# Kernel tuning notes

Hardware: AMD Instinct MI355X
Metric: run time of the kernel (lower is better)

Reference implementation:

```python
import jax, jax.numpy as jnp
import numpy as np

NUM_HEADS = 32
ROPE_BASE = 10000.0


def _rotate_half(x):
    h = x.shape[-1] // 2
    return jnp.concatenate([-x[..., h:], x[..., :h]], axis=-1)


def setup_inputs() -> dict:
    key = jax.random.key(0)
    ks = jax.random.split(key, 6)
    B, S, H = 2, 2048, 4096
    hidden_states = jax.random.normal(ks[0], (B, S, H), dtype=jnp.float32)
    # additive causal mask: 0 on/below diagonal, large negative above
    causal = jnp.tril(jnp.ones((S, S), dtype=bool))
    attention_mask = jnp.where(causal, 0.0, -1e9).astype(jnp.float32)
    attention_mask = jnp.broadcast_to(attention_mask[None, None], (B, 1, S, S))
    position_ids = jnp.broadcast_to(jnp.arange(S, dtype=jnp.int64 if jax.config.jax_enable_x64 else jnp.int32)[None, :], (B, S))
    scale = 1.0 / np.sqrt(H)
    Wq = jax.random.normal(ks[1], (H, H), dtype=jnp.float32) * scale
    Wk = jax.random.normal(ks[2], (H, H), dtype=jnp.float32) * scale
    Wv = jax.random.normal(ks[3], (H, H), dtype=jnp.float32) * scale
    Wo = jax.random.normal(ks[4], (H, H), dtype=jnp.float32) * scale
    return {"hidden_states": hidden_states, "attention_mask": attention_mask,
            "position_ids": position_ids, "Wq": Wq, "Wk": Wk, "Wv": Wv, "Wo": Wo}


def reference(hidden_states, attention_mask, position_ids, Wq, Wk, Wv, Wo):
    B, S, H = hidden_states.shape
    nh = NUM_HEADS
    hd = H // nh
    # QKV projections (torch Linear: y = x @ W.T), split heads -> [B, nh, S, hd]
    def proj(W):
        y = jnp.einsum('bsh,oh->bso', hidden_states, W)
        return y.reshape(B, S, nh, hd).transpose(0, 2, 1, 3)
    q, k, v = proj(Wq), proj(Wk), proj(Wv)
    # rotary embeddings gathered at position_ids
    inv_freq = 1.0 / (ROPE_BASE ** (jnp.arange(0, hd, 2, dtype=jnp.float32) / hd))
    freqs = position_ids.astype(jnp.float32)[:, :, None] * inv_freq[None, None, :]  # [B,S,hd/2]
    emb = jnp.concatenate([freqs, freqs], axis=-1)  # [B,S,hd]
    cos = jnp.cos(emb)[:, None, :, :]  # [B,1,S,hd]
    sin = jnp.sin(emb)[:, None, :, :]
    q = q * cos + _rotate_half(q) * sin
    k = k * cos + _rotate_half(k) * sin
    # scaled dot-product attention
    scores = jnp.einsum('bhqd,bhkd->bhqk', q, k) / jnp.sqrt(jnp.float32(hd))
    scores = scores + attention_mask
    scores = jnp.maximum(scores, jnp.finfo(scores.dtype).min)
    attn = jax.nn.softmax(scores, axis=-1)
    out = jnp.einsum('bhqk,bhkd->bhqd', attn, v)  # [B,nh,S,hd]
    out = out.transpose(0, 2, 1, 3).reshape(B, S, H)
    return jnp.einsum('bsh,oh->bso', out, Wo)
```

## Files before the change

### kernel.cpp

```cpp
#include <hip/hip_runtime.h>
#include <cstdint>
#include <cmath>

typedef __bf16 bf16;
typedef __bf16 bf16x8 __attribute__((ext_vector_type(8)));
typedef __bf16 bf16x4 __attribute__((ext_vector_type(4)));
typedef float f32x4 __attribute__((ext_vector_type(4)));

#define B_ 2
#define S_ 2048
#define H_ 4096
#define NH 32
#define HD 128

#define VMCNT(n) asm volatile("s_waitcnt vmcnt(" #n ")" ::: "memory")
#define BAR() __builtin_amdgcn_s_barrier()

__device__ __forceinline__ void gl_lds16(const void* g, void* l) {
  __builtin_amdgcn_global_load_lds(
      (const __attribute__((address_space(1))) unsigned int*)g,
      (__attribute__((address_space(3))) unsigned int*)l, 16, 0, 0);
}

__global__ __launch_bounds__(256) void cast_kernel(const float* __restrict__ in,
                                                   bf16* __restrict__ out, int n4) {
  int i = blockIdx.x * 256 + threadIdx.x;
  if (i < n4) {
    float4 v = ((const float4*)in)[i];
    bf16x4 o = {(bf16)v.x, (bf16)v.y, (bf16)v.z, (bf16)v.w};
    ((bf16x4*)out)[i] = o;
  }
}

template <int TM, int TN>
__device__ __forceinline__ void mfma_q(f32x4 (&acc)[8][4], bf16x8 (&a)[4][2],
                                       bf16x8 (&b)[2][2]) {
  __builtin_amdgcn_s_setprio(1);
#pragma unroll
  for (int i = 0; i < 4; ++i)
#pragma unroll
    for (int j = 0; j < 2; ++j)
#pragma unroll
      for (int kf = 0; kf < 2; ++kf)
        acc[TM * 4 + i][TN * 2 + j] = __builtin_amdgcn_mfma_f32_16x16x32_bf16(
            a[i][kf], b[j][kf], acc[TM * 4 + i][TN * 2 + j], 0, 0, 0);
  __builtin_amdgcn_s_setprio(0);
}

template <int EPI>
__global__ __launch_bounds__(512, 2) void gemm256(const bf16* __restrict__ A,
                                                  const bf16* __restrict__ Bw,
                                                  void* __restrict__ Cout) {
  constexpr int K = 4096, N = 4096, KT = K / 64;
  __shared__ __attribute__((aligned(16))) char lds[131072];
  char* Al = lds;
  char* Bl = lds + 65536;
  int tid = threadIdx.x;
  int l = tid & 63, lr = l & 15, lg = l >> 4;
  int w = tid >> 6, wm = w >> 2, wn = w & 3;
  int bid = (int)blockIdx.x;
  int swb = (bid & 7) * 32 + (bid >> 3);
  int r0 = (swb >> 4) * 256, c0 = (swb & 15) * 256;
  const bf16* Ab = A + (size_t)r0 * K;
  const bf16* Bb = Bw + (size_t)c0 * K;

  int lr0 = tid >> 3;
  int cel = (((tid & 7) ^ ((tid >> 3) & 7)) << 3);

  auto stageA = [&](int buf, int mh, int k0) {
    char* dst = Al + buf * 32768 + mh * 16384 + tid * 16;
    int ra = mh * 64 + lr0;
    gl_lds16(Ab + (size_t)ra * K + k0 + cel, dst);
    gl_lds16(Ab + (size_t)(ra + 128) * K + k0 + cel, dst + 8192);
  };
  auto stageB = [&](int buf, int nh, int k0) {
    char* dst = Bl + buf * 32768 + nh * 16384 + tid * 16;
    int n0 = (lr0 >> 5) * 64 + nh * 32 + (lr0 & 31);
    gl_lds16(Bb + (size_t)n0 * K + k0 + cel, dst);
    gl_lds16(Bb + (size_t)(n0 + 128) * K + k0 + cel, dst + 8192);
  };

  int rsw = (lr & 7) << 4;
  auto ldA = [&](bf16x8 (&dst)[4][2], int buf, int mh) {
    char* base = Al + buf * 32768 + mh * 16384 + wm * 8192;
#pragma unroll
    for (int mfl = 0; mfl < 4; ++mfl)
#pragma unroll
      for (int kf = 0; kf < 2; ++kf)
        __builtin_memcpy(&dst[mfl][kf],
                         base + (mfl * 16 + lr) * 128 + ((kf * 64 + lg * 16) ^ rsw), 16);
  };
  auto ldB = [&](bf16x8 (&dst)[2][2], int buf, int nh) {
    char* base = Bl + buf * 32768 + nh * 16384 + wn * 4096;
#pragma unroll
    for (int nfl = 0; nfl < 2; ++nfl)
#pragma unroll
      for (int kf = 0; kf < 2; ++kf)
        __builtin_memcpy(&dst[nfl][kf],
                         base + (nfl * 16 + lr) * 128 + ((kf * 64 + lg * 16) ^ rsw), 16);
  };

  bf16x8 af[4][2], bf0[2][2], bf1[2][2];
  f32x4 acc[8][4] = {};

  stageA(0, 0, 0);
  stageB(0, 0, 0);
  stageB(0, 1, 0);
  stageA(0, 1, 0);
  VMCNT(4); BAR();

  for (int kt = 0; kt < KT - 1; ++kt) {
    int buf = kt & 1, nb = buf ^ 1;
    int k0n = (kt + 1) * 64;
    ldA(af, buf, 0);
    ldB(bf0, buf, 0);
    stageA(nb, 0, k0n);
    mfma_q<0, 0>(acc, af, bf0);
    VMCNT(2); BAR();
    ldB(bf1, buf, 1);
    stageB(nb, 0, k0n);
    mfma_q<0, 1>(acc, af, bf1);
    ldA(af, buf, 1);
    stageB(nb, 1, k0n);
    mfma_q<1, 1>(acc, af, bf1);
    stageA(nb, 1, k0n);
    mfma_q<1, 0>(acc, af, bf0);
    VMCNT(4); BAR();
  }
  {
    int buf = (KT - 1) & 1;
    ldA(af, buf, 0);
    ldB(bf0, buf, 0);
    mfma_q<0, 0>(acc, af, bf0);
    VMCNT(2); BAR();
    ldB(bf1, buf, 1);
    mfma_q<0, 1>(acc, af, bf1);
    VMCNT(0); BAR();
    ldA(af, buf, 1);
    mfma_q<1, 1>(acc, af, bf1);
    mfma_q<1, 0>(acc, af, bf0);
  }

#pragma unroll
  for (int mf = 0; mf < 8; ++mf)
#pragma unroll
    for (int nf = 0; nf < 4; ++nf) {
      int orow = r0 + wm * 128 + mf * 16 + lg * 4;
      int ocol = c0 + wn * 64 + nf * 16 + lr;
      if (EPI == 0) {
        bf16* C = (bf16*)Cout;
#pragma unroll
        for (int jr = 0; jr < 4; ++jr)
          C[(size_t)(orow + jr) * N + ocol] = (bf16)acc[mf][nf][jr];
      } else {
        float* C = (float*)Cout;
#pragma unroll
        for (int jr = 0; jr < 4; ++jr)
          C[(size_t)(orow + jr) * N + ocol] = acc[mf][nf][jr];
      }
    }
}

__global__ __launch_bounds__(256) void rope_kernel(bf16* __restrict__ Qx,
                                                   bf16* __restrict__ Kx,
                                                   const int* __restrict__ pos,
                                                   float qscale) {
  int r = blockIdx.x;
  bf16* X = blockIdx.y ? Kx : Qx;
  float scale = blockIdx.y ? 1.0f : qscale;
  float pf = (float)pos[r];
  int i = threadIdx.x & 63;
  int h0 = threadIdx.x >> 6;
  float ang = pf * exp2f(-0.20762050593046868f * (float)i);
  float sn = sinf(ang), cs = cosf(ang);
  bf16* row = X + (size_t)r * H_;
#pragma unroll
  for (int h = h0; h < NH; h += 4) {
    bf16* p = row + h * HD + i;
    float a = (float)p[0], b = (float)p[64];
    p[0] = (bf16)((a * cs - b * sn) * scale);
    p[64] = (bf16)((b * cs + a * sn) * scale);
  }
}

__global__ __launch_bounds__(256) void transpose_v(const bf16* __restrict__ V,
                                                   bf16* __restrict__ Vt) {
  __shared__ __attribute__((aligned(16))) bf16 tile[64][130];
  int bh = blockIdx.y;
  int b = bh >> 5, h = bh & 31;
  int s0 = blockIdx.x * 64;
  int t = threadIdx.x;
  const bf16* src = V + (size_t)(b * S_ + s0) * H_ + h * HD;
  int rr = t >> 4, cc = (t & 15) * 8;
#pragma unroll
  for (int k = 0; k < 4; ++k) {
    bf16x8 v;
    __builtin_memcpy(&v, src + (size_t)(rr + k * 16) * H_ + cc, 16);
#pragma unroll
    for (int u = 0; u < 8; ++u) tile[rr + k * 16][cc + u] = v[u];
  }
  __syncthreads();
  bf16* dst = Vt + (size_t)bh * HD * S_;
  int sl = t & 63, d0 = t >> 6;
  for (int j = 0; j < 32; ++j) {
    int d = d0 + j * 4;
    dst[(size_t)d * S_ + s0 + sl] = tile[sl][d];
  }
}

__global__ __launch_bounds__(512, 4) void attn_kernel(const bf16* __restrict__ Q,
                                                      const bf16* __restrict__ Km,
                                                      const bf16* __restrict__ Vt,
                                                      bf16* __restrict__ Out) {
  __shared__ __attribute__((aligned(16))) bf16 Ks[2][64 * 128];
  __shared__ __attribute__((aligned(16))) bf16 Vs[2][128 * 64];
  __shared__ __attribute__((aligned(16))) bf16 P_lds[8][16 * 64];
  int tid = threadIdx.x;
  int w = tid >> 6, l = tid & 63;
  int lr = l & 15, lg = l >> 4;
  int f = (int)(blockIdx.y * gridDim.x + blockIdx.x);
  int wk = (f & 7) * 128 + (f >> 3);
  int bh = wk >> 4, b = bh >> 5, h = bh & 31;
  int qt = 15 - (wk & 15);
  int q0w = qt * 128 + w * 16;
  const bf16* Qb = Q + (size_t)b * S_ * H_ + h * HD;
  const char* Kg = (const char*)(Km + (size_t)b * S_ * H_ + h * HD);
  const char* Vg = (const char*)(Vt + (size_t)bh * HD * S_);
  bf16* Ob = Out + (size_t)b * S_ * H_ + h * HD;

  bf16x8 qf[4];
#pragma unroll
  for (int dk = 0; dk < 4; ++dk)
    __builtin_memcpy(&qf[dk], Qb + (size_t)(q0w + lr) * H_ + dk * 32 + lg * 8, 16);

  f32x4 o[8] = {};
  float m = -INFINITY, ls = 0.f;
  int nkv_blk = 2 * qt + 2;
  int nkv_w = 2 * qt + (w >> 2) + 1;

  auto stageK = [&](int buf, int kv0) {
#pragma unroll
    for (int p = 0; p < 2; ++p) {
      int row = p * 32 + (tid >> 4);
      int src = ((tid & 15) * 16) ^ ((row & 7) << 4);
      gl_lds16(Kg + (size_t)(kv0 + row) * (H_ * 2) + src,
               (char*)&Ks[buf][0] + p * 8192 + w * 1024);
    }
  };
  auto stageV = [&](int buf, int kv0) {
#pragma unroll
    for (int p = 0; p < 2; ++p) {
      int row = p * 64 + (tid >> 3);
      int src = ((tid & 7) * 16) ^ ((row & 7) << 4);
      gl_lds16(Vg + (size_t)row * (S_ * 2) + (size_t)kv0 * 2 + src,
               (char*)&Vs[buf][0] + p * 8192 + w * 1024);
    }
  };

  stageK(0, 0);
  stageV(0, 0);
  __syncthreads();

  int cur = 0;
  char* Pl = (char*)&P_lds[w][0];
  for (int t = 0; t < nkv_blk; ++t) {
    int kv0 = t * 64;
    if (t + 1 < nkv_blk) {
      stageK(cur ^ 1, kv0 + 64);
      stageV(cur ^ 1, kv0 + 64);
    }
    if (t < nkv_w) {
      const char* Kl = (const char*)&Ks[cur][0];
      const char* Vl = (const char*)&Vs[cur][0];
      f32x4 s4[4] = {};
      __builtin_amdgcn_s_setprio(1);
#pragma unroll
      for (int dk = 0; dk < 4; ++dk)
#pragma unroll
        for (int st = 0; st < 4; ++st) {
          int row = st * 16 + lr;
          int cb = (dk * 64 + lg * 16) ^ ((row & 7) << 4);
          bf16x8 kf;
          __builtin_memcpy(&kf, Kl + row * 256 + cb, 16);
          s4[st] = __builtin_amdgcn_mfma_f32_16x16x32_bf16(kf, qf[dk], s4[st], 0, 0, 0);
        }
      __builtin_amdgcn_s_setprio(0);
      if (t == nkv_w - 1) {
        int qg = q0w + lr;
#pragma unroll
        for (int st = 0; st < 4; ++st)
#pragma unroll
          for (int j = 0; j < 4; ++j)
            if (kv0 + st * 16 + lg * 4 + j > qg) s4[st][j] = -INFINITY;
      }
      float mx = -INFINITY;
#pragma unroll
      for (int st = 0; st < 4; ++st)
#pragma unroll
        for (int j = 0; j < 4; ++j) mx = fmaxf(mx, s4[st][j]);
      mx = fmaxf(mx, __shfl_xor(mx, 16));
      mx = fmaxf(mx, __shfl_xor(mx, 32));
      float sc = 1.0f;
      if (!__all((int)(mx <= m + 8.0f))) {
        float mn = fmaxf(m, mx);
        sc = exp2f(m - mn);
        m = mn;
        float scq0 = __shfl(sc, lg * 4 + 0);
        float scq1 = __shfl(sc, lg * 4 + 1);
        float scq2 = __shfl(sc, lg * 4 + 2);
        float scq3 = __shfl(sc, lg * 4 + 3);
#pragma unroll
        for (int dt = 0; dt < 8; ++dt) {
          o[dt][0] *= scq0; o[dt][1] *= scq1; o[dt][2] *= scq2; o[dt][3] *= scq3;
        }
      }
      float pv[4][4], rs = 0.f;
#pragma unroll
      for (int st = 0; st < 4; ++st)
#pragma unroll
        for (int j = 0; j < 4; ++j) {
          pv[st][j] = exp2f(s4[st][j] - m);
          rs += pv[st][j];
        }
      ls = ls * sc + rs;
#pragma unroll
      for (int st = 0; st < 4; ++st) {
        bf16x4 pk = {(bf16)pv[st][0], (bf16)pv[st][1], (bf16)pv[st][2], (bf16)pv[st][3]};
        *(bf16x4*)(Pl + lr * 128 + ((st * 32 + lg * 8) ^ ((lr & 7) << 4))) = pk;
      }
      bf16x8 pa[2];
#pragma unroll
      for (int ks = 0; ks < 2; ++ks)
        __builtin_memcpy(&pa[ks], Pl + lr * 128 + ((ks * 64 + lg * 16) ^ ((lr & 7) << 4)), 16);
      __builtin_amdgcn_s_setprio(1);
#pragma unroll
      for (int dt = 0; dt < 8; ++dt)
#pragma unroll
        for (int ks = 0; ks < 2; ++ks) {
          int row = dt * 16 + lr;
          int cb = (ks * 64 + lg * 16) ^ ((row & 7) << 4);
          bf16x8 vf;
          __builtin_memcpy(&vf, Vl + row * 128 + cb, 16);
          o[dt] = __builtin_amdgcn_mfma_f32_16x16x32_bf16(pa[ks], vf, o[dt], 0, 0, 0);
        }
      __builtin_amdgcn_s_setprio(0);
    }
    __syncthreads();
    cur ^= 1;
  }
  ls += __shfl_xor(ls, 16);
  ls += __shfl_xor(ls, 32);
  float lsq[4];
#pragma unroll
  for (int j = 0; j < 4; ++j) lsq[j] = __shfl(ls, lg * 4 + j);
#pragma unroll
  for (int j = 0; j < 4; ++j) {
    float inv = 1.0f / lsq[j];
#pragma unroll
    for (int dt = 0; dt < 8; ++dt)
      Ob[(size_t)(q0w + lg * 4 + j) * H_ + dt * 16 + lr] = (bf16)(o[dt][j] * inv);
  }
}

extern "C" void kernel_launch(void* const* d_in, const int* in_sizes, int n_in,
                              void* d_out, int out_size, void* d_ws, size_t ws_size,
                              hipStream_t stream) {
  const float* X = (const float*)d_in[0];
  const int* pos = (const int*)d_in[2];
  const float* Wq = (const float*)d_in[3];
  const float* Wk = (const float*)d_in[4];
  const float* Wv = (const float*)d_in[5];
  const float* Wo = (const float*)d_in[6];
  float* out = (float*)d_out;
  char* ws = (char*)d_ws;
  const size_t MB32 = 32ull << 20;
  bf16* Xb = (bf16*)ws;
  bf16* Wb = (bf16*)(ws + MB32);
  bf16* Qb = (bf16*)(ws + 2 * MB32);
  bf16* Kb = (bf16*)(ws + 3 * MB32);
  bf16* Vb = (bf16*)(ws + 4 * MB32);
  bf16* Vt = (bf16*)(ws + 5 * MB32);

  const int n4 = (4096 * 4096) / 4;
  dim3 cgrid(n4 / 256), cblk(256);
  dim3 ggrid(256), gblk(512);

  cast_kernel<<<cgrid, cblk, 0, stream>>>(X, Xb, n4);
  cast_kernel<<<cgrid, cblk, 0, stream>>>(Wq, Wb, n4);
  gemm256<0><<<ggrid, gblk, 0, stream>>>(Xb, Wb, Qb);
  cast_kernel<<<cgrid, cblk, 0, stream>>>(Wk, Wb, n4);
  gemm256<0><<<ggrid, gblk, 0, stream>>>(Xb, Wb, Kb);
  cast_kernel<<<cgrid, cblk, 0, stream>>>(Wv, Wb, n4);
  gemm256<0><<<ggrid, gblk, 0, stream>>>(Xb, Wb, Vb);

  const float qscale = 1.4426950408889634f / 11.313708498984760f;
  rope_kernel<<<dim3(4096, 2), 256, 0, stream>>>(Qb, Kb, pos, qscale);
  transpose_v<<<dim3(32, 64), 256, 0, stream>>>(Vb, Vt);

  attn_kernel<<<dim3(16, 64), 512, 0, stream>>>(Qb, Kb, Vt, Xb);

  cast_kernel<<<cgrid, cblk, 0, stream>>>(Wo, Wb, n4);
  gemm256<1><<<ggrid, gblk, 0, stream>>>(Xb, Wb, out);
}
```

Before: 822.6 us.

## Fuse Q/K/V projection GEMMs into one 768-block launch with grouped tile mapping

Casts Wk and Wv into spare buffers (the Vt workspace and the output buffer) up front so all three QKV weight matrices are in bf16 at once. A single 768-block GEMM then computes Q, K and V together, choosing weight and output per block by column group. The block-to-tile mapping is rebuilt so each group of 8 consecutive blocks shares A rows, and the staging order in the k-loop is shifted so both B halves are issued earlier, with the wait count relaxed to match. This removes two launches and the tail effects between them, and fills the GPU with three times as many blocks per wave. It reuses the output and Vt buffers as scratch before they are written later.

```diff
diff --git a/kernel.cpp b/kernel.cpp
--- a/kernel.cpp
+++ b/kernel.cpp
@@ -47,10 +47,14 @@
   __builtin_amdgcn_s_setprio(0);
 }
 
-template <int EPI>
+template <int EPI, int NC>
 __global__ __launch_bounds__(512, 2) void gemm256(const bf16* __restrict__ A,
-                                                  const bf16* __restrict__ Bw,
-                                                  void* __restrict__ Cout) {
+                                                  const bf16* __restrict__ B0g,
+                                                  const bf16* __restrict__ B1g,
+                                                  const bf16* __restrict__ B2g,
+                                                  void* __restrict__ C0g,
+                                                  void* __restrict__ C1g,
+                                                  void* __restrict__ C2g) {
   constexpr int K = 4096, N = 4096, KT = K / 64;
   __shared__ __attribute__((aligned(16))) char lds[131072];
   char* Al = lds;
@@ -59,8 +63,12 @@
   int l = tid & 63, lr = l & 15, lg = l >> 4;
   int w = tid >> 6, wm = w >> 2, wn = w & 3;
   int bid = (int)blockIdx.x;
-  int swb = (bid & 7) * 32 + (bid >> 3);
-  int r0 = (swb >> 4) * 256, c0 = (swb & 15) * 256;
+  int x = bid & 7, local = bid >> 3;
+  int lr0b = local / NC, lc0 = local % NC;
+  int r0 = (x * 2 + lr0b) * 256;
+  int g = lc0 >> 4;
+  int c0 = (lc0 & 15) * 256;
+  const bf16* Bw = (g == 0) ? B0g : ((g == 1) ? B1g : B2g);
   const bf16* Ab = A + (size_t)r0 * K;
   const bf16* Bb = Bw + (size_t)c0 * K;
 
@@ -115,15 +123,15 @@
     ldA(af, buf, 0);
     ldB(bf0, buf, 0);
     stageA(nb, 0, k0n);
+    stageB(nb, 0, k0n);
     mfma_q<0, 0>(acc, af, bf0);
-    VMCNT(2); BAR();
+    VMCNT(4); BAR();
     ldB(bf1, buf, 1);
-    stageB(nb, 0, k0n);
+    stageB(nb, 1, k0n);
     mfma_q<0, 1>(acc, af, bf1);
     ldA(af, buf, 1);
-    stageB(nb, 1, k0n);
+    stageA(nb, 1, k0n);
     mfma_q<1, 1>(acc, af, bf1);
-    stageA(nb, 1, k0n);
     mfma_q<1, 0>(acc, af, bf0);
     VMCNT(4); BAR();
   }
@@ -141,6 +149,7 @@
     mfma_q<1, 0>(acc, af, bf0);
   }
 
+  void* Cg = (g == 0) ? C0g : ((g == 1) ? C1g : C2g);
 #pragma unroll
   for (int mf = 0; mf < 8; ++mf)
 #pragma unroll
@@ -148,12 +157,12 @@
       int orow = r0 + wm * 128 + mf * 16 + lg * 4;
       int ocol = c0 + wn * 64 + nf * 16 + lr;
       if (EPI == 0) {
-        bf16* C = (bf16*)Cout;
+        bf16* C = (bf16*)Cg;
 #pragma unroll
         for (int jr = 0; jr < 4; ++jr)
           C[(size_t)(orow + jr) * N + ocol] = (bf16)acc[mf][nf][jr];
       } else {
-        float* C = (float*)Cout;
+        float* C = (float*)Cg;
 #pragma unroll
         for (int jr = 0; jr < 4; ++jr)
           C[(size_t)(orow + jr) * N + ocol] = acc[mf][nf][jr];
@@ -380,18 +389,17 @@
   bf16* Kb = (bf16*)(ws + 3 * MB32);
   bf16* Vb = (bf16*)(ws + 4 * MB32);
   bf16* Vt = (bf16*)(ws + 5 * MB32);
+  bf16* Wvb = (bf16*)d_out;
 
   const int n4 = (4096 * 4096) / 4;
   dim3 cgrid(n4 / 256), cblk(256);
-  dim3 ggrid(256), gblk(512);
 
   cast_kernel<<<cgrid, cblk, 0, stream>>>(X, Xb, n4);
   cast_kernel<<<cgrid, cblk, 0, stream>>>(Wq, Wb, n4);
-  gemm256<0><<<ggrid, gblk, 0, stream>>>(Xb, Wb, Qb);
-  cast_kernel<<<cgrid, cblk, 0, stream>>>(Wk, Wb, n4);
-  gemm256<0><<<ggrid, gblk, 0, stream>>>(Xb, Wb, Kb);
-  cast_kernel<<<cgrid, cblk, 0, stream>>>(Wv, Wb, n4);
-  gemm256<0><<<ggrid, gblk, 0, stream>>>(Xb, Wb, Vb);
+  cast_kernel<<<cgrid, cblk, 0, stream>>>(Wk, Vt, n4);
+  cast_kernel<<<cgrid, cblk, 0, stream>>>(Wv, Wvb, n4);
+
+  gemm256<0, 48><<<dim3(768), dim3(512), 0, stream>>>(Xb, Wb, Vt, Wvb, Qb, Kb, Vb);
 
   const float qscale = 1.4426950408889634f / 11.313708498984760f;
   rope_kernel<<<dim3(4096, 2), 256, 0, stream>>>(Qb, Kb, pos, qscale);
@@ -400,5 +408,5 @@
   attn_kernel<<<dim3(16, 64), 512, 0, stream>>>(Qb, Kb, Vt, Xb);
 
   cast_kernel<<<cgrid, cblk, 0, stream>>>(Wo, Wb, n4);
-  gemm256<1><<<ggrid, gblk, 0, stream>>>(Xb, Wb, out);
-}
+  gemm256<1, 16><<<dim3(256), dim3(512), 0, stream>>>(Xb, Wb, Wb, Wb, out, out, out);
+}
```

Result: faster. 762.6 us (-7.3%).
